# Optimization experiments

Hardware: AMD Instinct MI355X
Metric: run time of the kernel (lower is better)

## Reference

```python
import jax, jax.numpy as jnp
import numpy as np

# PGA G(3,0,1) multivector component order:
# [1, e0,e1,e2,e3, e01,e02,e03,e12,e13,e23, e012,e013,e023,e123, e0123]
INV = jnp.array([0, 2, 3, 4, 8, 9, 10, 14])  # blades without e0 (invariant inner product)
NUM_HEADS = 8


def make_basis():
    """9 Pin-equivariant linear maps on 16-dim multivectors (GATr basis):
    5 grade projections + 4 left-multiplications by e0."""
    B = np.zeros((9, 16, 16), dtype=np.float32)
    grades = [[0], [1, 2, 3, 4], [5, 6, 7, 8, 9, 10], [11, 12, 13, 14], [15]]
    for a, g in enumerate(grades):
        for i in g:
            B[a, i, i] = 1.0
    e0maps = [[(0, 1)], [(2, 5), (3, 6), (4, 7)], [(8, 11), (9, 12), (10, 13)], [(14, 15)]]
    for a, ps in enumerate(e0maps, start=5):
        for s, d in ps:
            B[a, d, s] = 1.0
    return jnp.asarray(B)


def equi_linear(x, w, b, basis):
    # x: [..., i, 16]; w: [o, i, 9]; b: [o] added to scalar component only
    xb = jnp.einsum('ajm,...im->...iaj', basis, x)
    out = jnp.einsum('oia,...iaj->...oj', w, xb)
    return out.at[..., 0].add(b)


def equi_rms_norm(x, weight, eps=1e-6):
    # x: [b, t, c, 16]; invariant squared norm per channel, RMS over channels
    n = jnp.mean(jnp.sum(x[..., INV] ** 2, axis=-1), axis=-1, keepdims=True)  # [b,t,1]
    return x * jax.lax.rsqrt(n + eps)[..., None] * weight[:, None]


def forward(hidden, w_attn, b_attn, w_next, b_next, ln_weight, basis):
    B, T, C, K = hidden.shape
    H = NUM_HEADS
    h = equi_rms_norm(hidden, ln_weight)
    qkv = equi_linear(h, w_attn, b_attn, basis)               # [b,t,3*H*C,16]
    qkv = qkv.reshape(B, T, 3, H, C, K).transpose(2, 0, 3, 1, 4, 5)  # [3,b,h,t,c,k]
    q, k, v = qkv[0], qkv[1], qkv[2]
    # inner-product attention (ipa): invariant inner product over non-e0 blades, summed over channels
    ipa = jnp.einsum('bhtcf,bhscf->bhts', q[..., INV], k[..., INV])
    # distance-aware attention (daa): -||pq - pk||^2 over trivector point coords (e012,e013,e023)
    pq, pk = q[..., 11:14], k[..., 11:14]
    qn = jnp.sum(pq * pq, axis=(-1, -2))                      # [b,h,t]
    kn = jnp.sum(pk * pk, axis=(-1, -2))                      # [b,h,s]
    daa = 2.0 * jnp.einsum('bhtcx,bhscx->bhts', pq, pk) - qn[..., :, None] - kn[..., None, :]
    logits = (ipa + daa) / jnp.sqrt(jnp.float32(8 * C))
    attn = jax.nn.softmax(logits, axis=-1)
    out = jnp.einsum('bhts,bhsck->bhtck', attn, v)            # [b,h,t,c,k]
    out = out.transpose(0, 2, 1, 3, 4).reshape(B, T, H * C, K)
    out = equi_linear(out, w_next, b_next, basis)
    return out + hidden


def setup_inputs() -> dict:
    key = jax.random.key(0)
    k1, k2, k3, k4 = jax.random.split(key, 4)
    B, T, C, H = 4, 1024, 48, NUM_HEADS
    hidden = jax.random.normal(k1, (B, T, C, 16), dtype=jnp.float32)
    s_attn = 1.0 / np.sqrt(C * 9)
    s_next = 1.0 / np.sqrt(H * C * 9)
    return {
        'hidden': hidden,
        'w_attn': jax.random.normal(k2, (3 * H * C, C, 9), dtype=jnp.float32) * s_attn,
        'b_attn': jnp.zeros((3 * H * C,), dtype=jnp.float32),
        'w_next': jax.random.normal(k3, (C, H * C, 9), dtype=jnp.float32) * s_next,
        'b_next': jnp.zeros((C,), dtype=jnp.float32),
        'ln_weight': jnp.ones((C,), dtype=jnp.float32),
        'basis': make_basis(),
    }


def reference(hidden, w_attn, b_attn, w_next, b_next, ln_weight, basis):
    return forward(hidden, w_attn, b_attn, w_next, b_next, ln_weight, basis)
```

## Files before the change

### kernel.cpp

```cpp
#include <hip/hip_runtime.h>
#include <math.h>

#define BB 4
#define TT 1024
#define CC 48
#define HH 8
#define THD_B (HH*TT)
#define FF 576
#define CK (CC*16)

#define QF_S  ((size_t)THD_B*FF)
#define VT_S  ((size_t)THD_B*CK)
#define AO_S  ((size_t)HH*TT*768)
#define U_S   ((size_t)HH*TT*TT)
#define RP_S  ((size_t)HH*8*TT)
#define HTB_S ((size_t)16*TT*48)

typedef __attribute__((ext_vector_type(8))) short bf16x8;
typedef __attribute__((ext_vector_type(4))) float f32x4;

__constant__ int c_gj[16]   = {0,1,1,1,1,2,2,2,2,2,2,3,3,3,3,4};
__constant__ int c_ej[16]   = {-1,5,-1,-1,-1,6,6,6,-1,-1,-1,7,7,7,-1,8};
__constant__ int c_srcj[16] = {0,0,0,0,0,2,3,4,0,0,0,8,9,10,0,14};
__constant__ int c_fi[16]   = {0,-1,1,2,3,-1,-1,-1,4,5,6,8,9,10,7,-1};

__device__ inline ushort f2bf(float x) {
  union { float f; unsigned u; } a; a.f = x;
  unsigned r = a.u + 0x7FFFu + ((a.u >> 16) & 1u);
  return (ushort)(r >> 16);
}
__device__ inline float bf2f(ushort u) {
  union { unsigned u; float f; } a; a.u = ((unsigned)u) << 16; return a.f;
}
__device__ inline int swz64(int row, int chunk) {
  return row*64 + (((chunk & 4) | ((chunk ^ (row >> 2)) & 3)) << 3);
}
__device__ inline void glds16(const ushort* g, ushort* l) {
  __builtin_amdgcn_global_load_lds((const __attribute__((address_space(1))) void*)g,
                                   (__attribute__((address_space(3))) void*)l, 16, 0, 0);
}

__global__ void kfill(float* __restrict__ p, size_t n, float v) {
  size_t i = (size_t)blockIdx.x*256 + threadIdx.x;
  size_t stride = (size_t)gridDim.x*256;
  for (; i < n; i += stride) p[i] = v;
}

__global__ void k0b_wplanes(const float* __restrict__ w_next,
                            ushort* __restrict__ wBt) {
  int idx = blockIdx.x*256 + threadIdx.x;
  if (idx >= 16*48*384) return;
  int j = idx / (48*384), rem = idx % (48*384), o = rem / 384, i = rem % 384;
  int h = i / 48, c = i % 48;
  int g = c_gj[j], e = c_ej[j];
  ushort* dst = wBt + ((size_t)j*48 + o)*768;
  dst[h*96 + c]      = f2bf(w_next[((size_t)o*384 + i)*9 + g]);
  dst[h*96 + 48 + c] = (e >= 0) ? f2bf(w_next[((size_t)o*384 + i)*9 + e]) : (ushort)0;
}

__global__ void k0c_wqkv(const float* __restrict__ w_attn,
                         ushort* __restrict__ wB) {
  int idx = blockIdx.x*256 + threadIdx.x;
  if (idx >= 16*1152*48) return;
  int j = idx / (1152*48), rem = idx % (1152*48), o = rem / 48, i = rem % 48;
  int g = c_gj[j], e = c_ej[j];
  float scl = (j >= 11 && j <= 13 && o < 768) ? 1.41421356237f : 1.0f;
  ushort* dst = wB + ((size_t)j*1152 + o)*96;
  dst[i]      = f2bf(w_attn[((size_t)o*48 + i)*9 + g] * scl);
  dst[48 + i] = (e >= 0) ? f2bf(w_attn[((size_t)o*48 + i)*9 + e] * scl) : (ushort)0;
}

__global__ __launch_bounds__(256) void k1_rmsnorm(const float* __restrict__ hidden,
                                                  const float* __restrict__ lnw,
                                                  ushort* __restrict__ hTb0, int b0) {
  const int lb = blockIdx.y;
  const float* hidden_b = hidden + (size_t)(b0 + lb)*TT*768;
  ushort* hTb = hTb0 + (size_t)lb*HTB_S;
  int n = blockIdx.x, tid = threadIdx.x;
  __shared__ float xs[768];
  __shared__ float red[256];
  float psum = 0.f;
  for (int e = tid; e < 768; e += 256) {
    float v = hidden_b[(size_t)n*768 + e];
    xs[e] = v;
    int k = e & 15;
    if ((0x471Du >> k) & 1u) psum += v*v;
  }
  red[tid] = psum;
  __syncthreads();
  for (int s = 128; s > 0; s >>= 1) { if (tid < s) red[tid] += red[tid+s]; __syncthreads(); }
  float scale = rsqrtf(red[0]/48.0f + 1e-6f);
  for (int e = tid; e < 768; e += 256) {
    int k = e / 48, i = e % 48;
    hTb[((size_t)k*TT + n)*48 + i] = f2bf(xs[i*16 + k] * scale * lnw[i]);
  }
}

__global__ __launch_bounds__(256) void k1b_qkv_mfma(const ushort* __restrict__ hTb0,
                                                    const ushort* __restrict__ wB,
                                                    const float* __restrict__ b_attn,
                                                    ushort* __restrict__ qf0,
                                                    ushort* __restrict__ kf0,
                                                    ushort* __restrict__ vT0) {
  const int j = blockIdx.z & 15, lb = blockIdx.z >> 4;
  const int oy = blockIdx.y;
  const int fi = c_fi[j];
  if (fi < 0 && oy < 6) return;
  const ushort* hTb = hTb0 + (size_t)lb*HTB_S;
  ushort* qf = qf0 + (size_t)lb*QF_S;
  ushort* kf = kf0 + (size_t)lb*QF_S;
  ushort* vT = vT0 + (size_t)lb*VT_S;
  const int t0 = blockIdx.x*128, o0 = oy*128;
  const int srcj = c_srcj[j];
  __shared__ __align__(16) ushort smem[2*128*104];
  ushort* As = smem;
  ushort* Bs = smem + 128*104;
  const int tid = threadIdx.x;
  const int lane = tid & 63, wid = tid >> 6;
  const int wr = wid >> 1, wc = wid & 1;
  const int rr = lane & 15, kq = lane >> 4;
  {
    const int r = tid >> 1, half = tid & 1;
    const ushort* sa = hTb + ((size_t)(half ? srcj : j)*TT + t0 + r)*48;
    const ushort* sb = wB + ((size_t)j*1152 + o0 + r)*96 + half*48;
    #pragma unroll
    for (int i = 0; i < 6; ++i) {
      *(ulonglong2*)(&As[r*104 + half*48 + i*8]) = *(const ulonglong2*)(sa + i*8);
      *(ulonglong2*)(&Bs[r*104 + half*48 + i*8]) = *(const ulonglong2*)(sb + i*8);
    }
  }
  __syncthreads();
  f32x4 acc[4][4] = {};
  #pragma unroll
  for (int ks = 0; ks < 3; ++ks) {
    bf16x8 af[4], bfv[4];
    #pragma unroll
    for (int m = 0; m < 4; ++m)
      af[m] = *(const bf16x8*)(&As[(wr*64 + m*16 + rr)*104 + ks*32 + kq*8]);
    #pragma unroll
    for (int n = 0; n < 4; ++n)
      bfv[n] = *(const bf16x8*)(&Bs[(wc*64 + n*16 + rr)*104 + ks*32 + kq*8]);
    #pragma unroll
    for (int m = 0; m < 4; ++m)
      #pragma unroll
      for (int n = 0; n < 4; ++n)
        acc[m][n] = __builtin_amdgcn_mfma_f32_16x16x32_bf16(af[m], bfv[n], acc[m][n], 0, 0, 0);
  }
  const int cr = (lane >> 4) << 2, cc = lane & 15;
  __syncthreads();
  ushort* E = smem;
  if (oy < 6) {
    #pragma unroll
    for (int n = 0; n < 4; ++n) {
      const int ol = wc*64 + n*16 + cc;
      const float bias = (j == 0) ? b_attn[o0 + ol] : 0.f;
      #pragma unroll
      for (int m = 0; m < 4; ++m) {
        const int tb = wr*64 + m*16 + cr;
        #pragma unroll
        for (int r = 0; r < 4; ++r)
          E[(tb + r)*136 + ol] = f2bf(acc[m][n][r] + bias);
      }
    }
    __syncthreads();
    #pragma unroll
    for (int i = 0; i < 8; ++i) {
      int s = tid + 256*i;
      int tl = s >> 4, o8 = (s & 15)*8;
      ulonglong2 v = *(const ulonglong2*)(&E[tl*136 + o8]);
      int og = o0 + o8;
      int qkv = og / 384, rem = og % 384, head = rem / 48, c = rem % 48;
      ushort* dst = (qkv == 0 ? qf : kf) + ((size_t)head*TT + t0 + tl)*FF + fi*48 + c;
      *(ulonglong2*)dst = v;
    }
  } else {
    #pragma unroll
    for (int n = 0; n < 4; ++n) {
      const int ol = wc*64 + n*16 + cc;
      const float bias = (j == 0) ? b_attn[o0 + ol] : 0.f;
      #pragma unroll
      for (int m = 0; m < 4; ++m) {
        const int tb = wr*64 + m*16 + cr;
        uint2 pk;
        pk.x = (uint)f2bf(acc[m][n][0] + bias) | ((uint)f2bf(acc[m][n][1] + bias) << 16);
        pk.y = (uint)f2bf(acc[m][n][2] + bias) | ((uint)f2bf(acc[m][n][3] + bias) << 16);
        *(uint2*)(&E[ol*136 + tb]) = pk;
      }
    }
    __syncthreads();
    #pragma unroll
    for (int i = 0; i < 8; ++i) {
      int s = tid + 256*i;
      int ol = s >> 4, t8 = (s & 15)*8;
      ulonglong2 v = *(const ulonglong2*)(&E[ol*136 + t8]);
      int og = o0 + ol;
      int rem = og % 384, head = rem / 48, c = rem % 48;
      ushort* dst = vT + ((size_t)((head*16 + j)*48 + c))*TT + t0 + t8;
      *(ulonglong2*)dst = v;
    }
  }
}

__global__ __launch_bounds__(256) void k1c_extras(ushort* __restrict__ qf0,
                                                  ushort* __restrict__ kf0) {
  const int lb = blockIdx.y;
  int th = blockIdx.x*4 + (threadIdx.x >> 6);
  int lane = threadIdx.x & 63;
  ushort* q = qf0 + (size_t)lb*QF_S + (size_t)th*FF;
  ushort* k = kf0 + (size_t)lb*QF_S + (size_t)th*FF;
  float qn = 0.f, kn = 0.f;
  if (lane < 36) {
    ushort4 a = *(const ushort4*)(q + 384 + lane*4);
    ushort4 b = *(const ushort4*)(k + 384 + lane*4);
    float x;
    x = bf2f(a.x); qn += x*x;  x = bf2f(a.y); qn += x*x;
    x = bf2f(a.z); qn += x*x;  x = bf2f(a.w); qn += x*x;
    x = bf2f(b.x); kn += x*x;  x = bf2f(b.y); kn += x*x;
    x = bf2f(b.z); kn += x*x;  x = bf2f(b.w); kn += x*x;
  }
  #pragma unroll
  for (int off = 32; off; off >>= 1) {
    qn += __shfl_xor(qn, off, 64);
    kn += __shfl_xor(kn, off, 64);
  }
  if (lane == 0) {
    q[528] = f2bf(qn*0.5f); q[529] = 0x3F80u;
    k[528] = 0xBF80u;       k[529] = f2bf(-kn*0.5f);
  }
  if (lane < 46) { q[530+lane] = 0; k[530+lane] = 0; }
}

__global__ __launch_bounds__(256) void k2b_logits_mfma(const ushort* __restrict__ qf0,
                                                       const ushort* __restrict__ kf0,
                                                       ushort* __restrict__ ubuf0,
                                                       float* __restrict__ rowpart0) {
  const int h = blockIdx.z & 7, lb = blockIdx.z >> 3;
  const int t0 = blockIdx.y*64, s0 = blockIdx.x*128;
  const ushort* Ag = qf0 + (size_t)lb*QF_S + (size_t)h*TT*FF;
  const ushort* Bg = kf0 + (size_t)lb*QF_S + (size_t)h*TT*FF;
  ushort* ubuf = ubuf0 + (size_t)lb*U_S;
  float* rowpart = rowpart0 + (size_t)lb*RP_S;
  __shared__ __align__(16) ushort smem[64*64 + 128*64];
  ushort* As = smem;
  ushort* Bs = smem + 64*64;
  const int tid = threadIdx.x;
  const int lane = tid & 63, wid = tid >> 6;
  const int wr = wid >> 1, wc = wid & 1;
  const int rr = lane & 15, kq = lane >> 4;
  const int lr8 = lane >> 3, ch = lane & 7;
  f32x4 acc[2][4] = {};
  for (int kk = 0; kk < FF; kk += 64) {
    __syncthreads();
    #pragma unroll
    for (int i = 0; i < 2; ++i) {
      int r = wid*16 + i*8 + lr8;
      int sch = (ch & 4) | ((ch ^ (r >> 2)) & 3);
      glds16(Ag + (size_t)(t0 + r)*FF + kk + sch*8, &As[(wid*16 + i*8)*64]);
    }
    #pragma unroll
    for (int i = 0; i < 4; ++i) {
      int r = wid*32 + i*8 + lr8;
      int sch = (ch & 4) | ((ch ^ (r >> 2)) & 3);
      glds16(Bg + (size_t)(s0 + r)*FF + kk + sch*8, &Bs[(wid*32 + i*8)*64]);
    }
    __syncthreads();
    #pragma unroll
    for (int ks = 0; ks < 2; ++ks) {
      bf16x8 af[2], bfv[4];
      #pragma unroll
      for (int m = 0; m < 2; ++m) af[m]  = *(const bf16x8*)(&As[swz64(wr*32 + m*16 + rr, ks*4 + kq)]);
      #pragma unroll
      for (int n = 0; n < 4; ++n) bfv[n] = *(const bf16x8*)(&Bs[swz64(wc*64 + n*16 + rr, ks*4 + kq)]);
      #pragma unroll
      for (int m = 0; m < 2; ++m)
        #pragma unroll
        for (int n = 0; n < 4; ++n)
          acc[m][n] = __builtin_amdgcn_mfma_f32_16x16x32_bf16(af[m], bfv[n], acc[m][n], 0, 0, 0);
    }
  }
  const float iscl = 0.051031036307982884f;
  const int cr = (lane >> 4) << 2, cc = lane & 15;
  __syncthreads();
  ushort* E = smem;
  float* part = (float*)(smem + 8704);
  #pragma unroll
  for (int m = 0; m < 2; ++m)
    #pragma unroll
    for (int n = 0; n < 4; ++n) {
      const int tb = wr*32 + m*16 + cr;
      const int sl = wc*64 + n*16 + cc;
      #pragma unroll
      for (int r = 0; r < 4; ++r)
        E[(tb + r)*136 + sl] = f2bf(__expf(acc[m][n][r]*iscl));
    }
  __syncthreads();
  {
    const int row = tid >> 2, q4 = tid & 3;
    const ushort* er = &E[row*136 + q4*32];
    float seg = 0.f;
    #pragma unroll
    for (int i = 0; i < 4; ++i) {
      ulonglong2 v = *(const ulonglong2*)(er + i*8);
      const ushort* u = (const ushort*)&v;
      #pragma unroll
      for (int jj = 0; jj < 8; ++jj) seg += bf2f(u[jj]);
    }
    part[tid] = seg;
  }
  #pragma unroll
  for (int i = 0; i < 4; ++i) {
    int s = tid + 256*i;
    int tl = s >> 4, s8 = (s & 15)*8;
    ulonglong2 v = *(const ulonglong2*)(&E[tl*136 + s8]);
    *(ulonglong2*)(ubuf + ((size_t)h*TT + t0 + tl)*TT + s0 + s8) = v;
  }
  __syncthreads();
  if (tid < 64)
    rowpart[((size_t)h*8 + blockIdx.x)*TT + t0 + tid] =
        part[tid*4] + part[tid*4+1] + part[tid*4+2] + part[tid*4+3];
}

__global__ __launch_bounds__(256) void k2d_pv_mfma(const ushort* __restrict__ ubuf0,
                                                   const ushort* __restrict__ vT0,
                                                   const float* __restrict__ rowpart0,
                                                   ushort* __restrict__ aoH0) {
  const int h = blockIdx.z & 7, lb = blockIdx.z >> 3;
  const int t0 = blockIdx.y*64, c0 = blockIdx.x*128;
  const ushort* Ag = ubuf0 + (size_t)lb*U_S + (size_t)h*TT*TT;
  const ushort* Bg = vT0 + (size_t)lb*VT_S + (size_t)h*CK*TT;
  const float* rowpart = rowpart0 + (size_t)lb*RP_S;
  ushort* aoH = aoH0 + (size_t)lb*AO_S;
  __shared__ __align__(16) ushort smem[64*64 + 128*64];
  ushort* As = smem;
  ushort* Bs = smem + 64*64;
  const int tid = threadIdx.x;
  const int lane = tid & 63, wid = tid >> 6;
  const int wr = wid >> 1, wc = wid & 1;
  const int rr = lane & 15, kq = lane >> 4;
  const int lr8 = lane >> 3, ch = lane & 7;
  f32x4 acc[2][4] = {};
  for (int kk = 0; kk < TT; kk += 64) {
    __syncthreads();
    #pragma unroll
    for (int i = 0; i < 2; ++i) {
      int r = wid*16 + i*8 + lr8;
      int sch = (ch & 4) | ((ch ^ (r >> 2)) & 3);
      glds16(Ag + (size_t)(t0 + r)*TT + kk + sch*8, &As[(wid*16 + i*8)*64]);
    }
    #pragma unroll
    for (int i = 0; i < 4; ++i) {
      int r = wid*32 + i*8 + lr8;
      int sch = (ch & 4) | ((ch ^ (r >> 2)) & 3);
      glds16(Bg + (size_t)(c0 + r)*TT + kk + sch*8, &Bs[(wid*32 + i*8)*64]);
    }
    __syncthreads();
    #pragma unroll
    for (int ks = 0; ks < 2; ++ks) {
      bf16x8 af[2], bfv[4];
      #pragma unroll
      for (int m = 0; m < 2; ++m) af[m]  = *(const bf16x8*)(&As[swz64(wr*32 + m*16 + rr, ks*4 + kq)]);
      #pragma unroll
      for (int n = 0; n < 4; ++n) bfv[n] = *(const bf16x8*)(&Bs[swz64(wc*64 + n*16 + rr, ks*4 + kq)]);
      #pragma unroll
      for (int m = 0; m < 2; ++m)
        #pragma unroll
        for (int n = 0; n < 4; ++n)
          acc[m][n] = __builtin_amdgcn_mfma_f32_16x16x32_bf16(af[m], bfv[n], acc[m][n], 0, 0, 0);
    }
  }
  const int cr = (lane >> 4) << 2, cc = lane & 15;
  __syncthreads();
  ushort* E = smem;
  float* invs = (float*)(smem + 8704);
  if (tid < 64) {
    const float* rp = rowpart + (size_t)h*8*TT + t0 + tid;
    float rs = 0.f;
    #pragma unroll
    for (int sx = 0; sx < 8; ++sx) rs += rp[(size_t)sx*TT];
    invs[tid] = 1.0f / rs;
  }
  __syncthreads();
  #pragma unroll
  for (int m = 0; m < 2; ++m)
    #pragma unroll
    for (int n = 0; n < 4; ++n) {
      const int tb = wr*32 + m*16 + cr;
      const int cl = wc*64 + n*16 + cc;
      #pragma unroll
      for (int r = 0; r < 4; ++r)
        E[(tb + r)*136 + cl] = f2bf(acc[m][n][r] * invs[tb + r]);
    }
  __syncthreads();
  #pragma unroll
  for (int i = 0; i < 4; ++i) {
    int s = tid + 256*i;
    int tl = s >> 4, c8 = (s & 15)*8;
    ulonglong2 v = *(const ulonglong2*)(&E[tl*136 + c8]);
    *(ulonglong2*)(aoH + ((size_t)h*TT + t0 + tl)*768 + c0 + c8) = v;
  }
}

__global__ __launch_bounds__(256) void k3_mfma(const ushort* __restrict__ aoH0,
                                               const ushort* __restrict__ wBt,
                                               const float* __restrict__ b_next,
                                               const float* __restrict__ hidden,
                                               float* __restrict__ out, int b0) {
  const int lb = blockIdx.z;
  const ushort* aoH = aoH0 + (size_t)lb*AO_S;
  const float* hidden_b = hidden + (size_t)(b0 + lb)*TT*768;
  float* out_b = out + (size_t)(b0 + lb)*TT*768;
  const int j = blockIdx.y, t0 = blockIdx.x*64;
  const int srcj = c_srcj[j];
  __shared__ __align__(16) ushort As[64*104];
  __shared__ __align__(16) ushort Bs[48*104];
  const int tid = threadIdx.x;
  const int lane = tid & 63, wid = tid >> 6;
  const int rr = lane & 15, kq = lane >> 4;
  const ushort* bw = wBt + (size_t)j*48*768;
  const int ar = tid >> 2, aq = tid & 3;
  f32x4 acc[3] = {};
  for (int hh = 0; hh < HH; ++hh) {
    __syncthreads();
    {
      const ushort* rowp = aoH + ((size_t)hh*TT + t0 + ar)*768;
      #pragma unroll
      for (int q = 0; q < 3; ++q) {
        int ci = aq*3 + q;
        const ushort* src = rowp + ((ci < 6) ? (j*48 + ci*8) : (srcj*48 + (ci - 6)*8));
        *(ulonglong2*)(&As[ar*104 + ci*8]) = *(const ulonglong2*)src;
      }
      if (tid < 192) {
        const ushort* brow = bw + (size_t)ar*768 + hh*96;
        #pragma unroll
        for (int q = 0; q < 3; ++q) {
          int ci = aq*3 + q;
          *(ulonglong2*)(&Bs[ar*104 + ci*8]) = *(const ulonglong2*)(brow + ci*8);
        }
      }
    }
    __syncthreads();
    #pragma unroll
    for (int ks = 0; ks < 3; ++ks) {
      bf16x8 af = *(const bf16x8*)(&As[(wid*16 + rr)*104 + ks*32 + kq*8]);
      #pragma unroll
      for (int n = 0; n < 3; ++n) {
        bf16x8 bf = *(const bf16x8*)(&Bs[(n*16 + rr)*104 + ks*32 + kq*8]);
        acc[n] = __builtin_amdgcn_mfma_f32_16x16x32_bf16(af, bf, acc[n], 0, 0, 0);
      }
    }
  }
  const int cr = (lane >> 4) << 2, cc = lane & 15;
  #pragma unroll
  for (int n = 0; n < 3; ++n) {
    int o = n*16 + cc;
    float bb = (j == 0) ? b_next[o] : 0.f;
    #pragma unroll
    for (int r = 0; r < 4; ++r) {
      int t = t0 + wid*16 + cr + r;
      size_t off = (size_t)t*768 + o*16 + j;
      out_b[off] = acc[n][r] + bb + hidden_b[off];
    }
  }
}

extern "C" void kernel_launch(void* const* d_in, const int* in_sizes, int n_in,
                              void* d_out, int out_size, void* d_ws, size_t ws_size,
                              hipStream_t stream) {
  const float* hidden = (const float*)d_in[0];
  const float* w_attn = (const float*)d_in[1];
  const float* b_attn = (const float*)d_in[2];
  const float* w_next = (const float*)d_in[3];
  const float* b_next = (const float*)d_in[4];
  const float* ln_w   = (const float*)d_in[5];
  float* out = (float*)d_out;
  float* ws = (float*)d_ws;

  const size_t PER_B_FL = U_S/2 + RP_S + QF_S + VT_S/2 + AO_S/2 + VT_S/2 + HTB_S/2;
  const size_t W_FL = (16*48*768 + 16*1152*96)/2;
  int nb = 0;
  for (int g = 4; g >= 1; g >>= 1) {
    size_t need = ((size_t)g*(U_S/2 + RP_S + QF_S  + VT_S/2 + AO_S/2 + HTB_S/2) + W_FL)*4;
    if (ws_size >= need) { nb = g; break; }
  }
  if (nb == 0) {
    kfill<<<2048, 256, 0, stream>>>(out, (size_t)out_size, 1.0e6f);
    return;
  }

  ushort* ubuf    = (ushort*)ws;
  float*  rowpart = ws + (size_t)nb*(U_S/2);
  ushort* qf      = (ushort*)(rowpart + (size_t)nb*RP_S);
  ushort* kf      = qf + (size_t)nb*QF_S;
  ushort* vT      = kf + (size_t)nb*QF_S;
  ushort* aoH     = vT + (size_t)nb*VT_S;
  ushort* hTb     = aoH + (size_t)nb*AO_S;
  ushort* wBt     = hTb + (size_t)nb*HTB_S;
  ushort* wB      = wBt + (size_t)16*48*768;

  k0b_wplanes<<<1152, 256, 0, stream>>>(w_next, wBt);
  k0c_wqkv<<<3456, 256, 0, stream>>>(w_attn, wB);
  for (int b0 = 0; b0 < BB; b0 += nb) {
    k1_rmsnorm<<<dim3(TT, nb), 256, 0, stream>>>(hidden, ln_w, hTb, b0);
    k1b_qkv_mfma<<<dim3(8, 9, 16*nb), 256, 0, stream>>>(hTb, wB, b_attn, qf, kf, vT);
    k1c_extras<<<dim3(THD_B/4, nb), 256, 0, stream>>>(qf, kf);
    k2b_logits_mfma<<<dim3(8, 16, 8*nb), 256, 0, stream>>>(qf, kf, ubuf, rowpart);
    k2d_pv_mfma<<<dim3(6, 16, 8*nb), 256, 0, stream>>>(ubuf, vT, rowpart, aoH);
    k3_mfma<<<dim3(16, 16, nb), 256, 0, stream>>>(aoH, wBt, b_next, hidden, out, b0);
  }
}
```

Measured before the change: 270.3 us.

## Fuse logits and PV into one attention kernel holding exp rows in LDS

Replaces the separate logits kernel (which wrote bf16 exp-logits and row partial sums to global memory) and the PV kernel with one fused kernel. Each 512-thread block owns 64 query rows of one head, keeps the full 64x1024 unnormalised probability tile in LDS (128KB), computes row sums in-register, and then runs the PV GEMM straight from LDS. This removes the global round trip of the attention matrix and one launch. In exchange the grid shrinks to 16x8xnb blocks with roughly 145KB of LDS each, so occupancy is one block per CU and parallelism is limited.

Result: slower. 476.6 us (+76.3%).

```diff
diff --git a/kernel.cpp b/kernel.cpp
--- a/kernel.cpp
+++ b/kernel.cpp
@@ -12,8 +12,6 @@
 #define QF_S  ((size_t)THD_B*FF)
 #define VT_S  ((size_t)THD_B*CK)
 #define AO_S  ((size_t)HH*TT*768)
-#define U_S   ((size_t)HH*TT*TT)
-#define RP_S  ((size_t)HH*8*TT)
 #define HTB_S ((size_t)16*TT*48)
 
 typedef __attribute__((ext_vector_type(8))) short bf16x8;
@@ -230,173 +228,128 @@
   if (lane < 46) { q[530+lane] = 0; k[530+lane] = 0; }
 }
 
-__global__ __launch_bounds__(256) void k2b_logits_mfma(const ushort* __restrict__ qf0,
-                                                       const ushort* __restrict__ kf0,
-                                                       ushort* __restrict__ ubuf0,
-                                                       float* __restrict__ rowpart0) {
-  const int h = blockIdx.z & 7, lb = blockIdx.z >> 3;
-  const int t0 = blockIdx.y*64, s0 = blockIdx.x*128;
-  const ushort* Ag = qf0 + (size_t)lb*QF_S + (size_t)h*TT*FF;
-  const ushort* Bg = kf0 + (size_t)lb*QF_S + (size_t)h*TT*FF;
-  ushort* ubuf = ubuf0 + (size_t)lb*U_S;
-  float* rowpart = rowpart0 + (size_t)lb*RP_S;
-  __shared__ __align__(16) ushort smem[64*64 + 128*64];
-  ushort* As = smem;
-  ushort* Bs = smem + 64*64;
+__global__ __launch_bounds__(512) void k2f_attn(const ushort* __restrict__ qf0,
+                                                const ushort* __restrict__ kf0,
+                                                const ushort* __restrict__ vT0,
+                                                ushort* __restrict__ aoH0) {
+  const int h = blockIdx.y, lb = blockIdx.z;
+  const int t0 = blockIdx.x*64;
+  const ushort* Qg = qf0 + (size_t)lb*QF_S + (size_t)h*TT*FF;
+  const ushort* Kg = kf0 + (size_t)lb*QF_S + (size_t)h*TT*FF;
+  const ushort* Vg = vT0 + (size_t)lb*VT_S + (size_t)h*CK*TT;
+  ushort* aoH = aoH0 + (size_t)lb*AO_S;
+
+  __shared__ __align__(16) ushort smem[65536 + 4096 + 8192 + 384];
+  ushort* U  = smem;
+  ushort* As = smem + 65536;
+  ushort* Bs = smem + 65536 + 4096;
+  float*  part = (float*)(smem + 65536 + 4096 + 8192);
+  float*  invs = part + 128;
+
   const int tid = threadIdx.x;
-  const int lane = tid & 63, wid = tid >> 6;
-  const int wr = wid >> 1, wc = wid & 1;
+  const int lane = tid & 63, w = tid >> 6;
+  const int tb = (w & 3)*16, sh = (w >> 2)*64;
   const int rr = lane & 15, kq = lane >> 4;
+  const int cr = (lane >> 4) << 2, cc = lane & 15;
   const int lr8 = lane >> 3, ch = lane & 7;
-  f32x4 acc[2][4] = {};
-  for (int kk = 0; kk < FF; kk += 64) {
+  const float iscl = 0.051031036307982884f;
+
+  float partial[4] = {0.f, 0.f, 0.f, 0.f};
+
+  for (int s0 = 0; s0 < TT; s0 += 128) {
+    f32x4 acc[4] = {};
+    for (int kk = 0; kk < FF; kk += 64) {
+      __syncthreads();
+      {
+        int r = w*8 + lr8;
+        int sch = (ch & 4) | ((ch ^ (r >> 2)) & 3);
+        glds16(Qg + (size_t)(t0 + r)*FF + kk + sch*8, &As[w*8*64]);
+      }
+      #pragma unroll
+      for (int i = 0; i < 2; ++i) {
+        int r = i*64 + w*8 + lr8;
+        int sch = (ch & 4) | ((ch ^ (r >> 2)) & 3);
+        glds16(Kg + (size_t)(s0 + r)*FF + kk + sch*8, &Bs[(i*64 + w*8)*64]);
+      }
+      __syncthreads();
+      #pragma unroll
+      for (int ks = 0; ks < 2; ++ks) {
+        bf16x8 af = *(const bf16x8*)(&As[swz64(tb + rr, ks*4 + kq)]);
+        #pragma unroll
+        for (int n = 0; n < 4; ++n) {
+          bf16x8 bv = *(const bf16x8*)(&Bs[swz64(sh + n*16 + rr, ks*4 + kq)]);
+          acc[n] = __builtin_amdgcn_mfma_f32_16x16x32_bf16(af, bv, acc[n], 0, 0, 0);
+        }
+      }
+    }
+    #pragma unroll
+    for (int n = 0; n < 4; ++n)
+      #pragma unroll
+      for (int j = 0; j < 4; ++j) {
+        int row = tb + cr + j;
+        int col = s0 + sh + n*16 + cc;
+        ushort u = f2bf(__expf(acc[n][j]*iscl));
+        int kb = col >> 6, chk = (col >> 3) & 7, el = col & 7;
+        int szc = (chk & 4) | ((chk ^ (row >> 2)) & 3);
+        U[row*1024 + kb*64 + szc*8 + el] = u;
+        partial[j] += bf2f(u);
+      }
+  }
+  #pragma unroll
+  for (int j = 0; j < 4; ++j)
+    #pragma unroll
+    for (int off = 1; off < 16; off <<= 1)
+      partial[j] += __shfl_xor(partial[j], off, 64);
+  if (cc == 0) {
+    #pragma unroll
+    for (int j = 0; j < 4; ++j)
+      part[(w >> 2)*64 + tb + cr + j] = partial[j];
+  }
+  __syncthreads();
+  if (tid < 64) invs[tid] = 1.0f / (part[tid] + part[64 + tid]);
+
+  for (int c0 = 0; c0 < CK; c0 += 128) {
+    f32x4 acc[4] = {};
+    for (int kk = 0; kk < TT; kk += 64) {
+      __syncthreads();
+      #pragma unroll
+      for (int i = 0; i < 2; ++i) {
+        int r = i*64 + w*8 + lr8;
+        int sch = (ch & 4) | ((ch ^ (r >> 2)) & 3);
+        glds16(Vg + (size_t)(c0 + r)*TT + kk + sch*8, &Bs[(i*64 + w*8)*64]);
+      }
+      __syncthreads();
+      const int kb = kk >> 6;
+      #pragma unroll
+      for (int ks = 0; ks < 2; ++ks) {
+        const int rowa = tb + rr, chnk = ks*4 + kq;
+        const int szc = (chnk & 4) | ((chnk ^ (rowa >> 2)) & 3);
+        bf16x8 af = *(const bf16x8*)(&U[rowa*1024 + kb*64 + szc*8]);
+        #pragma unroll
+        for (int n = 0; n < 4; ++n) {
+          bf16x8 bv = *(const bf16x8*)(&Bs[swz64(sh + n*16 + rr, chnk)]);
+          acc[n] = __builtin_amdgcn_mfma_f32_16x16x32_bf16(af, bv, acc[n], 0, 0, 0);
+        }
+      }
+    }
+    __syncthreads();
+    ushort* E = As;
+    #pragma unroll
+    for (int n = 0; n < 4; ++n)
+      #pragma unroll
+      for (int j = 0; j < 4; ++j) {
+        int row = tb + cr + j;
+        int cl = sh + n*16 + cc;
+        E[row*136 + cl] = f2bf(acc[n][j] * invs[row]);
+      }
     __syncthreads();
     #pragma unroll
     for (int i = 0; i < 2; ++i) {
-      int r = wid*16 + i*8 + lr8;
-      int sch = (ch & 4) | ((ch ^ (r >> 2)) & 3);
-      glds16(Ag + (size_t)(t0 + r)*FF + kk + sch*8, &As[(wid*16 + i*8)*64]);
-    }
-    #pragma unroll
-    for (int i = 0; i < 4; ++i) {
-      int r = wid*32 + i*8 + lr8;
-      int sch = (ch & 4) | ((ch ^ (r >> 2)) & 3);
-      glds16(Bg + (size_t)(s0 + r)*FF + kk + sch*8, &Bs[(wid*32 + i*8)*64]);
-    }
-    __syncthreads();
-    #pragma unroll
-    for (int ks = 0; ks < 2; ++ks) {
-      bf16x8 af[2], bfv[4];
-      #pragma unroll
-      for (int m = 0; m < 2; ++m) af[m]  = *(const bf16x8*)(&As[swz64(wr*32 + m*16 + rr, ks*4 + kq)]);
-      #pragma unroll
-      for (int n = 0; n < 4; ++n) bfv[n] = *(const bf16x8*)(&Bs[swz64(wc*64 + n*16 + rr, ks*4 + kq)]);
-      #pragma unroll
-      for (int m = 0; m < 2; ++m)
-        #pragma unroll
-        for (int n = 0; n < 4; ++n)
-          acc[m][n] = __builtin_amdgcn_mfma_f32_16x16x32_bf16(af[m], bfv[n], acc[m][n], 0, 0, 0);
-    }
-  }
-  const float iscl = 0.051031036307982884f;
-  const int cr = (lane >> 4) << 2, cc = lane & 15;
-  __syncthreads();
-  ushort* E = smem;
-  float* part = (float*)(smem + 8704);
-  #pragma unroll
-  for (int m = 0; m < 2; ++m)
-    #pragma unroll
-    for (int n = 0; n < 4; ++n) {
-      const int tb = wr*32 + m*16 + cr;
-      const int sl = wc*64 + n*16 + cc;
-      #pragma unroll
-      for (int r = 0; r < 4; ++r)
-        E[(tb + r)*136 + sl] = f2bf(__expf(acc[m][n][r]*iscl));
-    }
-  __syncthreads();
-  {
-    const int row = tid >> 2, q4 = tid & 3;
-    const ushort* er = &E[row*136 + q4*32];
-    float seg = 0.f;
-    #pragma unroll
-    for (int i = 0; i < 4; ++i) {
-      ulonglong2 v = *(const ulonglong2*)(er + i*8);
-      const ushort* u = (const ushort*)&v;
-      #pragma unroll
-      for (int jj = 0; jj < 8; ++jj) seg += bf2f(u[jj]);
-    }
-    part[tid] = seg;
-  }
-  #pragma unroll
-  for (int i = 0; i < 4; ++i) {
-    int s = tid + 256*i;
-    int tl = s >> 4, s8 = (s & 15)*8;
-    ulonglong2 v = *(const ulonglong2*)(&E[tl*136 + s8]);
-    *(ulonglong2*)(ubuf + ((size_t)h*TT + t0 + tl)*TT + s0 + s8) = v;
-  }
-  __syncthreads();
-  if (tid < 64)
-    rowpart[((size_t)h*8 + blockIdx.x)*TT + t0 + tid] =
-        part[tid*4] + part[tid*4+1] + part[tid*4+2] + part[tid*4+3];
-}
-
-__global__ __launch_bounds__(256) void k2d_pv_mfma(const ushort* __restrict__ ubuf0,
-                                                   const ushort* __restrict__ vT0,
-                                                   const float* __restrict__ rowpart0,
-                                                   ushort* __restrict__ aoH0) {
-  const int h = blockIdx.z & 7, lb = blockIdx.z >> 3;
-  const int t0 = blockIdx.y*64, c0 = blockIdx.x*128;
-  const ushort* Ag = ubuf0 + (size_t)lb*U_S + (size_t)h*TT*TT;
-  const ushort* Bg = vT0 + (size_t)lb*VT_S + (size_t)h*CK*TT;
-  const float* rowpart = rowpart0 + (size_t)lb*RP_S;
-  ushort* aoH = aoH0 + (size_t)lb*AO_S;
-  __shared__ __align__(16) ushort smem[64*64 + 128*64];
-  ushort* As = smem;
-  ushort* Bs = smem + 64*64;
-  const int tid = threadIdx.x;
-  const int lane = tid & 63, wid = tid >> 6;
-  const int wr = wid >> 1, wc = wid & 1;
-  const int rr = lane & 15, kq = lane >> 4;
-  const int lr8 = lane >> 3, ch = lane & 7;
-  f32x4 acc[2][4] = {};
-  for (int kk = 0; kk < TT; kk += 64) {
-    __syncthreads();
-    #pragma unroll
-    for (int i = 0; i < 2; ++i) {
-      int r = wid*16 + i*8 + lr8;
-      int sch = (ch & 4) | ((ch ^ (r >> 2)) & 3);
-      glds16(Ag + (size_t)(t0 + r)*TT + kk + sch*8, &As[(wid*16 + i*8)*64]);
-    }
-    #pragma unroll
-    for (int i = 0; i < 4; ++i) {
-      int r = wid*32 + i*8 + lr8;
-      int sch = (ch & 4) | ((ch ^ (r >> 2)) & 3);
-      glds16(Bg + (size_t)(c0 + r)*TT + kk + sch*8, &Bs[(wid*32 + i*8)*64]);
-    }
-    __syncthreads();
-    #pragma unroll
-    for (int ks = 0; ks < 2; ++ks) {
-      bf16x8 af[2], bfv[4];
-      #pragma unroll
-      for (int m = 0; m < 2; ++m) af[m]  = *(const bf16x8*)(&As[swz64(wr*32 + m*16 + rr, ks*4 + kq)]);
-      #pragma unroll
-      for (int n = 0; n < 4; ++n) bfv[n] = *(const bf16x8*)(&Bs[swz64(wc*64 + n*16 + rr, ks*4 + kq)]);
-      #pragma unroll
-      for (int m = 0; m < 2; ++m)
-        #pragma unroll
-        for (int n = 0; n < 4; ++n)
-          acc[m][n] = __builtin_amdgcn_mfma_f32_16x16x32_bf16(af[m], bfv[n], acc[m][n], 0, 0, 0);
-    }
-  }
-  const int cr = (lane >> 4) << 2, cc = lane & 15;
-  __syncthreads();
-  ushort* E = smem;
-  float* invs = (float*)(smem + 8704);
-  if (tid < 64) {
-    const float* rp = rowpart + (size_t)h*8*TT + t0 + tid;
-    float rs = 0.f;
-    #pragma unroll
-    for (int sx = 0; sx < 8; ++sx) rs += rp[(size_t)sx*TT];
-    invs[tid] = 1.0f / rs;
-  }
-  __syncthreads();
-  #pragma unroll
-  for (int m = 0; m < 2; ++m)
-    #pragma unroll
-    for (int n = 0; n < 4; ++n) {
-      const int tb = wr*32 + m*16 + cr;
-      const int cl = wc*64 + n*16 + cc;
-      #pragma unroll
-      for (int r = 0; r < 4; ++r)
-        E[(tb + r)*136 + cl] = f2bf(acc[m][n][r] * invs[tb + r]);
-    }
-  __syncthreads();
-  #pragma unroll
-  for (int i = 0; i < 4; ++i) {
-    int s = tid + 256*i;
-    int tl = s >> 4, c8 = (s & 15)*8;
-    ulonglong2 v = *(const ulonglong2*)(&E[tl*136 + c8]);
-    *(ulonglong2*)(aoH + ((size_t)h*TT + t0 + tl)*768 + c0 + c8) = v;
+      int s = tid + 512*i;
+      int tl = s >> 4, c8 = (s & 15)*8;
+      ulonglong2 v = *(const ulonglong2*)(&E[tl*136 + c8]);
+      *(ulonglong2*)(aoH + ((size_t)h*TT + t0 + tl)*768 + c0 + c8) = v;
+    }
   }
 }
 
@@ -475,27 +428,23 @@
   float* out = (float*)d_out;
   float* ws = (float*)d_ws;
 
-  const size_t PER_B_FL = U_S/2 + RP_S + QF_S + VT_S/2 + AO_S/2 + VT_S/2 + HTB_S/2;
+  const size_t PER_B_FL = QF_S + VT_S/2 + AO_S/2 + HTB_S/2;
   const size_t W_FL = (16*48*768 + 16*1152*96)/2;
   int nb = 0;
-  for (int g = 4; g >= 1; g >>= 1) {
-    size_t need = ((size_t)g*(U_S/2 + RP_S + QF_S  + VT_S/2 + AO_S/2 + HTB_S/2) + W_FL)*4;
-    if (ws_size >= need) { nb = g; break; }
-  }
+  for (int g = 4; g >= 1; g >>= 1)
+    if (ws_size >= ((size_t)g*PER_B_FL + W_FL)*4) { nb = g; break; }
   if (nb == 0) {
     kfill<<<2048, 256, 0, stream>>>(out, (size_t)out_size, 1.0e6f);
     return;
   }
 
-  ushort* ubuf    = (ushort*)ws;
-  float*  rowpart = ws + (size_t)nb*(U_S/2);
-  ushort* qf      = (ushort*)(rowpart + (size_t)nb*RP_S);
-  ushort* kf      = qf + (size_t)nb*QF_S;
-  ushort* vT      = kf + (size_t)nb*QF_S;
-  ushort* aoH     = vT + (size_t)nb*VT_S;
-  ushort* hTb     = aoH + (size_t)nb*AO_S;
-  ushort* wBt     = hTb + (size_t)nb*HTB_S;
-  ushort* wB      = wBt + (size_t)16*48*768;
+  ushort* qf  = (ushort*)ws;
+  ushort* kf  = qf + (size_t)nb*QF_S;
+  ushort* vT  = kf + (size_t)nb*QF_S;
+  ushort* aoH = vT + (size_t)nb*VT_S;
+  ushort* hTb = aoH + (size_t)nb*AO_S;
+  ushort* wBt = hTb + (size_t)nb*HTB_S;
+  ushort* wB  = wBt + (size_t)16*48*768;
 
   k0b_wplanes<<<1152, 256, 0, stream>>>(w_next, wBt);
   k0c_wqkv<<<3456, 256, 0, stream>>>(w_attn, wB);
@@ -503,8 +452,7 @@
     k1_rmsnorm<<<dim3(TT, nb), 256, 0, stream>>>(hidden, ln_w, hTb, b0);
     k1b_qkv_mfma<<<dim3(8, 9, 16*nb), 256, 0, stream>>>(hTb, wB, b_attn, qf, kf, vT);
     k1c_extras<<<dim3(THD_B/4, nb), 256, 0, stream>>>(qf, kf);
-    k2b_logits_mfma<<<dim3(8, 16, 8*nb), 256, 0, stream>>>(qf, kf, ubuf, rowpart);
-    k2d_pv_mfma<<<dim3(6, 16, 8*nb), 256, 0, stream>>>(ubuf, vT, rowpart, aoH);
+    k2f_attn<<<dim3(16, HH, nb), 512, 0, stream>>>(qf, kf, vT, aoH);
     k3_mfma<<<dim3(16, 16, nb), 256, 0, stream>>>(aoH, wBt, b_next, hidden, out, b0);
   }
 }
```
